# Performance work log

Measured on AMD Instinct MI355X. Metric: run time of the kernel, lower is better.

## Reference

```python
import jax, jax.numpy as jnp
import numpy as np

N_ATOMS = 400000   # total atoms in batch
N_MODELS = 4       # number of elements / sub-models
N_POINTS = 512     # inducing points per GPR
N_DESC = 32        # descriptor length


def setup_inputs() -> dict:
    key = jax.random.key(0)
    k1, k2, k3, k4 = jax.random.split(key, 4)
    element = jax.random.randint(k1, (N_ATOMS,), 0, N_MODELS, dtype=jnp.int32)
    x = jax.random.normal(k2, (N_ATOMS, N_DESC), dtype=jnp.float32)
    inducing_x = jax.random.normal(k3, (N_MODELS, N_POINTS, N_DESC), dtype=jnp.float32)
    alpha = jax.random.normal(k4, (N_MODELS, N_POINTS), dtype=jnp.float32)
    # torch code initializes lengthscales to -1 (log-space) with ARD (one per descriptor)
    log_ls = -jnp.ones((N_MODELS, N_DESC), dtype=jnp.float32)
    return {"element": element, "x": x, "inducing_x": inducing_x,
            "alpha": alpha, "log_ls": log_ls}


def _gpr_energies(x, Zm, am, log_lsm):
    """InducedKernelGPR.forward for one sub-model over ALL atoms.

    dist[p, n] = sum_d (x[n,d] - Z[p,d])^2 / exp(log_ls[d])
    out[n]     = sum_p alpha[p] * exp(-dist[p, n])

    Uses ||a-b||^2 = ||a||^2 + ||b||^2 - 2 a.b on 1/sqrt(ls)-scaled features
    to avoid materializing the [P, N, D] difference tensor.
    """
    inv_sqrt_ls = jnp.exp(-0.5 * log_lsm)          # [D]
    xs = x * inv_sqrt_ls                            # [N, D]
    zs = Zm * inv_sqrt_ls                           # [P, D]
    x2 = jnp.sum(xs * xs, axis=-1)                  # [N]
    z2 = jnp.sum(zs * zs, axis=-1)                  # [P]
    cross = jnp.einsum('pd,nd->pn', zs, xs)         # [P, N]
    dist = z2[:, None] + x2[None, :] - 2.0 * cross  # [P, N]
    return am @ jnp.exp(-dist)                      # [N]


def reference(element, x, inducing_x, alpha, log_ls):
    # Hard routing: each atom gets the prediction of the model matching its element.
    # Loop over the small fixed set of sub-models (structurally distinct params);
    # combine with a mask instead of dynamic-shape gather/scatter (jit-friendly).
    out = jnp.zeros(x.shape[0], dtype=x.dtype)
    for m in range(inducing_x.shape[0]):
        e_m = _gpr_energies(x, inducing_x[m], alpha[m], log_ls[m])  # [N]
        out = jnp.where(element == m, e_m, out)
    return out
```

## Files before the change

### kernel.cpp

```cpp
#include <hip/hip_runtime.h>
#include <math.h>

#define NA 400000
#define NM 4
#define NP 512
#define ND 32
#define SQF 1.6986437f
#define NBH 391
#define GTPB 512
#define NBLK 1024
#define WPM ((NBLK / NM) * 8)
#define ACUT 60.0f

typedef __attribute__((ext_vector_type(8))) _Float16 f16x8;
typedef __attribute__((ext_vector_type(4))) float f32x4;

#define WS_ZH   0
#define WS_AZY  131072
#define WS_BET  139264
#define WS_ISL  147456
#define WS_PART 147968
#define WS_CNT  154224
#define WS_BKT  154240

__global__ void prep_hist_kernel(const float* __restrict__ Z,
                                 const float* __restrict__ alpha,
                                 const float* __restrict__ lls,
                                 const int* __restrict__ el,
                                 unsigned short* __restrict__ zh_w,
                                 float* __restrict__ azy,
                                 float* __restrict__ bet,
                                 float* __restrict__ isl,
                                 int* __restrict__ part)
{
    __shared__ float isl_s[ND];
    __shared__ int h[16][NM];
    int tid = threadIdx.x;
    if (blockIdx.x < NM) {
        int m = blockIdx.x;
        if (tid < ND) {
            float v = expf(-0.5f * lls[m * ND + tid]) * SQF;
            isl_s[tid] = v;
            isl[m * ND + tid] = v;
        }
        __syncthreads();
        for (int p = tid; p < NP; p += blockDim.x) {
            const float* zp = Z + (size_t)(m * NP + p) * ND;
            int t = p >> 4, pl = p & 15;
            size_t fb = (size_t)(m * 32 + t) * 512;
            float z2 = 0.f;
#pragma unroll
            for (int d = 0; d < ND; ++d) {
                float zs = zp[d] * isl_s[d];
                _Float16 zh = (_Float16)zs;
                float zr = (float)zh;
                z2 = fmaf(zr, zr, z2);
                int lane = pl + 16 * (d >> 3), j = d & 7;
                zh_w[fb + lane * 8 + j] = __builtin_bit_cast(unsigned short, zh);
            }
            azy[m * NP + p] = -0.5f * z2;
            bet[m * NP + p] = alpha[m * NP + p] * 8.673617379884035e-19f;
        }
    } else {
        int wnd = blockIdx.x - NM;
        int wv = tid >> 6, lane = tid & 63;
        int i = wnd * 1024 + tid;
        int e = (i < NA) ? el[i] : -1;
#pragma unroll
        for (int mm = 0; mm < NM; ++mm) {
            unsigned long long b = __ballot(e == mm);
            if (lane == 0) h[wv][mm] = __popcll(b);
        }
        __syncthreads();
        if (tid < NM) {
            int s = 0;
#pragma unroll
            for (int k = 0; k < 16; ++k) s += h[k][tid];
            part[wnd * 4 + tid] = s;
        }
    }
}

__global__ void scatter_kernel(const int* __restrict__ el,
                               const int* __restrict__ part,
                               int* __restrict__ cnt,
                               int* __restrict__ bucket)
{
    __shared__ int wcnt_s[16][NM];
    __shared__ int wvoff_s[16][NM];
    __shared__ int gbase_s[NM];
    __shared__ int tot_s[NM];
    __shared__ int bw_s[NM];
    int b = blockIdx.x, tid = threadIdx.x;
    int wv = tid >> 6, lane = tid & 63;
    int i = b * 1024 + tid;
    int e = (i < NA) ? el[i] : -1;
    unsigned long long lt = (1ULL << lane) - 1ULL;
    int myrank = 0;
#pragma unroll
    for (int mm = 0; mm < NM; ++mm) {
        unsigned long long bl = __ballot(e == mm);
        if (e == mm) myrank = __popcll(bl & lt);
        if (lane == 0) wcnt_s[wv][mm] = __popcll(bl);
    }
    if (wv == 0) {
        int t0 = 0, t1 = 0, t2 = 0, t3 = 0, b0 = 0, b1 = 0, b2 = 0, b3 = 0;
        for (int w2 = lane; w2 < NBH; w2 += 64) {
            int4 pv = ((const int4*)part)[w2];
            t0 += pv.x; t1 += pv.y; t2 += pv.z; t3 += pv.w;
            if (w2 < b) { b0 += pv.x; b1 += pv.y; b2 += pv.z; b3 += pv.w; }
        }
#pragma unroll
        for (int s = 1; s < 64; s <<= 1) {
            t0 += __shfl_xor(t0, s); t1 += __shfl_xor(t1, s);
            t2 += __shfl_xor(t2, s); t3 += __shfl_xor(t3, s);
            b0 += __shfl_xor(b0, s); b1 += __shfl_xor(b1, s);
            b2 += __shfl_xor(b2, s); b3 += __shfl_xor(b3, s);
        }
        if (lane == 0) {
            tot_s[0] = t0; tot_s[1] = t1; tot_s[2] = t2; tot_s[3] = t3;
            bw_s[0] = b0; bw_s[1] = b1; bw_s[2] = b2; bw_s[3] = b3;
        }
    }
    __syncthreads();
    if (tid < NM) {
        int g = bw_s[tid];
        for (int mm = 0; mm < NM; ++mm) if (mm < tid) g += tot_s[mm];
        gbase_s[tid] = g;
        int run = 0;
#pragma unroll
        for (int k = 0; k < 16; ++k) { wvoff_s[k][tid] = run; run += wcnt_s[k][tid]; }
        if (b == 0) cnt[tid] = tot_s[tid];
    }
    __syncthreads();
    if (e >= 0) bucket[gbase_s[e] + wvoff_s[wv][e] + myrank] = i;
}

static __device__ __forceinline__ void build_frags(
    const float* __restrict__ x, const int* __restrict__ bucket,
    int base, int c, int wbase, int ll, int k0, float4 w0, float4 w1,
    f16x8* Bh, float* x2lc)
{
#pragma unroll
    for (int nt = 0; nt < 4; ++nt) {
        int j = wbase + nt * 16 + ll;
        int n = bucket[base + ((j < c) ? j : (c - 1))];
        const float4* xp = (const float4*)(x + (size_t)n * ND + k0);
        float4 a = xp[0], b = xp[1];
        float xs[8] = {a.x * w0.x, a.y * w0.y, a.z * w0.z, a.w * w0.w,
                       b.x * w1.x, b.y * w1.y, b.z * w1.z, b.w * w1.w};
        float s2 = 0.f;
#pragma unroll
        for (int i = 0; i < 8; ++i) {
            _Float16 xh = (_Float16)xs[i];
            Bh[nt][i] = xh;
            float xr = (float)xh;
            s2 = fmaf(xr, xr, s2);
        }
        s2 += __shfl_xor(s2, 16);
        s2 += __shfl_xor(s2, 32);
        x2lc[nt] = 0.5f * s2 - ACUT;
    }
}

__global__ __launch_bounds__(GTPB, 4)
void gpr_kernel(const float* __restrict__ x,
                const int* __restrict__ bucket,
                const unsigned short* __restrict__ zh_w,
                const float* __restrict__ azy_w,
                const float* __restrict__ bet_w,
                const float* __restrict__ isl_w,
                const int* __restrict__ cnt_w,
                float* __restrict__ out)
{
    __shared__ __align__(16) unsigned short zf[32][512];
    __shared__ __align__(16) float azy_s[NP];
    __shared__ __align__(16) float bet_s[NP];

    int m = blockIdx.x & 3;
    int tid = threadIdx.x;
    int c0 = cnt_w[0], c1 = cnt_w[1], c2 = cnt_w[2], c3 = cnt_w[3];
    int c    = (m == 0) ? c0 : (m == 1) ? c1 : (m == 2) ? c2 : c3;
    int base = (m == 0) ? 0 : (m == 1) ? c0 : (m == 2) ? c0 + c1 : c0 + c1 + c2;

    int wv = tid >> 6, lane = tid & 63;
    int lg = lane >> 4, ll = lane & 15;
    int k0 = lg * 8;
    int wm = (blockIdx.x >> 2) * 8 + wv;

    const float4* wp = (const float4*)(isl_w + m * ND + k0);
    float4 w0 = wp[0], w1 = wp[1];

    {
        const int4* zg = (const int4*)(zh_w + (size_t)m * 16384);
        int4* zs = (int4*)&zf[0][0];
#pragma unroll
        for (int i = 0; i < 4; ++i) zs[tid + i * GTPB] = zg[tid + i * GTPB];
        if (tid < 128)
            ((float4*)azy_s)[tid] = ((const float4*)(azy_w + m * NP))[tid];
        else if (tid < 256)
            ((float4*)bet_s)[tid - 128] = ((const float4*)(bet_w + m * NP))[tid - 128];
    }

    f16x8 Bh[4];
    float x2lc[4];
    bool active = (wm * 64 < c);
    if (active)
        build_frags(x, bucket, base, c, wm * 64, ll, k0, w0, w1, Bh, x2lc);

    __syncthreads();

    for (int s = wm; s * 64 < c; s += WPM) {
        int wbase = s * 64;
        if (s != wm)
            build_frags(x, bucket, base, c, wbase, ll, k0, w0, w1, Bh, x2lc);

        float acc[4] = {0.f, 0.f, 0.f, 0.f};

        f16x8 Ah = *(const f16x8*)&zf[0][lane * 8];
        float4 di = *(const float4*)&azy_s[4 * lg];
        float4 bi = *(const float4*)&bet_s[4 * lg];

#pragma unroll 2
        for (int t = 0; t < 32; ++t) {
            f16x8 AhC = Ah;
            f32x4 dinit = __builtin_bit_cast(f32x4, di);
            float4 be4 = bi;
            int tn = (t + 1) & 31;
            Ah = *(const f16x8*)&zf[tn][lane * 8];
            di = *(const float4*)&azy_s[tn * 16 + 4 * lg];
            bi = *(const float4*)&bet_s[tn * 16 + 4 * lg];

            f32x4 dd[4];
            __builtin_amdgcn_s_setprio(1);
#pragma unroll
            for (int nt = 0; nt < 4; ++nt)
                dd[nt] = __builtin_amdgcn_mfma_f32_16x16x32_f16(AhC, Bh[nt], dinit, 0, 0, 0);
            __builtin_amdgcn_s_setprio(0);

#pragma unroll
            for (int nt = 0; nt < 4; ++nt) {
                f32x4 d = dd[nt];
                float mx = fmaxf(fmaxf(d[0], d[1]), fmaxf(d[2], d[3]));
                if (__any(mx >= x2lc[nt])) {
                    float xl = x2lc[nt];
                    acc[nt] = fmaf(be4.x, __builtin_amdgcn_exp2f(d[0] - xl), acc[nt]);
                    acc[nt] = fmaf(be4.y, __builtin_amdgcn_exp2f(d[1] - xl), acc[nt]);
                    acc[nt] = fmaf(be4.z, __builtin_amdgcn_exp2f(d[2] - xl), acc[nt]);
                    acc[nt] = fmaf(be4.w, __builtin_amdgcn_exp2f(d[3] - xl), acc[nt]);
                }
            }
        }

#pragma unroll
        for (int nt = 0; nt < 4; ++nt) {
            float v = acc[nt];
            v += __shfl_xor(v, 16);
            v += __shfl_xor(v, 32);
            if (lane < 16) {
                int j = wbase + nt * 16 + lane;
                if (j < c) out[bucket[base + j]] = v;
            }
        }
    }
}

extern "C" void kernel_launch(void* const* d_in, const int* in_sizes, int n_in,
                              void* d_out, int out_size, void* d_ws, size_t ws_size,
                              hipStream_t stream)
{
    const int*   element    = (const int*)d_in[0];
    const float* x          = (const float*)d_in[1];
    const float* inducing_x = (const float*)d_in[2];
    const float* alpha      = (const float*)d_in[3];
    const float* log_ls     = (const float*)d_in[4];
    float* out = (float*)d_out;

    char* ws = (char*)d_ws;
    unsigned short* zh = (unsigned short*)(ws + WS_ZH);
    float* azy  = (float*)(ws + WS_AZY);
    float* bet  = (float*)(ws + WS_BET);
    float* isl  = (float*)(ws + WS_ISL);
    int*   part = (int*)(ws + WS_PART);
    int*   cnt  = (int*)(ws + WS_CNT);
    int*   bkt  = (int*)(ws + WS_BKT);

    (void)in_sizes; (void)n_in; (void)out_size; (void)ws_size;

    prep_hist_kernel<<<NM + NBH, 1024, 0, stream>>>(inducing_x, alpha, log_ls, element,
                                                    zh, azy, bet, isl, part);
    scatter_kernel<<<NBH, 1024, 0, stream>>>(element, part, cnt, bkt);
    gpr_kernel<<<NBLK, GTPB, 0, stream>>>(x, bkt, zh, azy, bet, isl, cnt, out);
}
```

Measured before the change: 44.01 us.

## Process 16-atom subtiles sequentially with software-prefetched x loads

Restructures the per-wave work so that, instead of holding four 16-atom B fragments and issuing four MFMAs per inducing-point step, each wave handles one 16-atom subtile at a time. The x row for the next subtile is prefetched into registers while the current one runs its 32-step MFMA/exp loop. This cuts register pressure and hides gather latency. In exchange each MFMA now has to wait on its own dependent exp chain, and the LDS reads of Z, azy and beta are repeated four times per 64-atom tile.

```diff
diff --git a/kernel.cpp b/kernel.cpp
--- a/kernel.cpp
+++ b/kernel.cpp
@@ -136,33 +136,6 @@
     if (e >= 0) bucket[gbase_s[e] + wvoff_s[wv][e] + myrank] = i;
 }
 
-static __device__ __forceinline__ void build_frags(
-    const float* __restrict__ x, const int* __restrict__ bucket,
-    int base, int c, int wbase, int ll, int k0, float4 w0, float4 w1,
-    f16x8* Bh, float* x2lc)
-{
-#pragma unroll
-    for (int nt = 0; nt < 4; ++nt) {
-        int j = wbase + nt * 16 + ll;
-        int n = bucket[base + ((j < c) ? j : (c - 1))];
-        const float4* xp = (const float4*)(x + (size_t)n * ND + k0);
-        float4 a = xp[0], b = xp[1];
-        float xs[8] = {a.x * w0.x, a.y * w0.y, a.z * w0.z, a.w * w0.w,
-                       b.x * w1.x, b.y * w1.y, b.z * w1.z, b.w * w1.w};
-        float s2 = 0.f;
-#pragma unroll
-        for (int i = 0; i < 8; ++i) {
-            _Float16 xh = (_Float16)xs[i];
-            Bh[nt][i] = xh;
-            float xr = (float)xh;
-            s2 = fmaf(xr, xr, s2);
-        }
-        s2 += __shfl_xor(s2, 16);
-        s2 += __shfl_xor(s2, 32);
-        x2lc[nt] = 0.5f * s2 - ACUT;
-    }
-}
-
 __global__ __launch_bounds__(GTPB, 4)
 void gpr_kernel(const float* __restrict__ x,
                 const int* __restrict__ bucket,
@@ -202,59 +175,75 @@
             ((float4*)bet_s)[tid - 128] = ((const float4*)(bet_w + m * NP))[tid - 128];
     }
 
-    f16x8 Bh[4];
-    float x2lc[4];
+    float4 ra, rb;
     bool active = (wm * 64 < c);
-    if (active)
-        build_frags(x, bucket, base, c, wm * 64, ll, k0, w0, w1, Bh, x2lc);
+    if (active) {
+        int j = wm * 64 + ll;
+        int n = bucket[base + ((j < c) ? j : (c - 1))];
+        const float4* xp = (const float4*)(x + (size_t)n * ND + k0);
+        ra = xp[0]; rb = xp[1];
+    }
 
     __syncthreads();
 
     for (int s = wm; s * 64 < c; s += WPM) {
         int wbase = s * 64;
-        if (s != wm)
-            build_frags(x, bucket, base, c, wbase, ll, k0, w0, w1, Bh, x2lc);
-
-        float acc[4] = {0.f, 0.f, 0.f, 0.f};
-
-        f16x8 Ah = *(const f16x8*)&zf[0][lane * 8];
-        float4 di = *(const float4*)&azy_s[4 * lg];
-        float4 bi = *(const float4*)&bet_s[4 * lg];
+        if (s != wm) {
+            int j = wbase + ll;
+            int n = bucket[base + ((j < c) ? j : (c - 1))];
+            const float4* xp = (const float4*)(x + (size_t)n * ND + k0);
+            ra = xp[0]; rb = xp[1];
+        }
+
+        for (int nt = 0; nt < 4; ++nt) {
+            float xs[8] = {ra.x * w0.x, ra.y * w0.y, ra.z * w0.z, ra.w * w0.w,
+                           rb.x * w1.x, rb.y * w1.y, rb.z * w1.z, rb.w * w1.w};
+            f16x8 B;
+            float s2 = 0.f;
+#pragma unroll
+            for (int i = 0; i < 8; ++i) {
+                _Float16 xh = (_Float16)xs[i];
+                B[i] = xh;
+                float xr = (float)xh;
+                s2 = fmaf(xr, xr, s2);
+            }
+            s2 += __shfl_xor(s2, 16);
+            s2 += __shfl_xor(s2, 32);
+            float x2lc = 0.5f * s2 - ACUT;
+
+            if (nt < 3) {
+                int j = wbase + (nt + 1) * 16 + ll;
+                int n = bucket[base + ((j < c) ? j : (c - 1))];
+                const float4* xp = (const float4*)(x + (size_t)n * ND + k0);
+                ra = xp[0]; rb = xp[1];
+            }
+
+            float acc = 0.f;
+            f16x8 Ah = *(const f16x8*)&zf[0][lane * 8];
+            float4 di = *(const float4*)&azy_s[4 * lg];
+            float4 bi = *(const float4*)&bet_s[4 * lg];
 
 #pragma unroll 2
-        for (int t = 0; t < 32; ++t) {
-            f16x8 AhC = Ah;
-            f32x4 dinit = __builtin_bit_cast(f32x4, di);
-            float4 be4 = bi;
-            int tn = (t + 1) & 31;
-            Ah = *(const f16x8*)&zf[tn][lane * 8];
-            di = *(const float4*)&azy_s[tn * 16 + 4 * lg];
-            bi = *(const float4*)&bet_s[tn * 16 + 4 * lg];
-
-            f32x4 dd[4];
-            __builtin_amdgcn_s_setprio(1);
-#pragma unroll
-            for (int nt = 0; nt < 4; ++nt)
-                dd[nt] = __builtin_amdgcn_mfma_f32_16x16x32_f16(AhC, Bh[nt], dinit, 0, 0, 0);
-            __builtin_amdgcn_s_setprio(0);
-
-#pragma unroll
-            for (int nt = 0; nt < 4; ++nt) {
-                f32x4 d = dd[nt];
+            for (int t = 0; t < 32; ++t) {
+                f16x8 AhC = Ah;
+                f32x4 dinit = __builtin_bit_cast(f32x4, di);
+                float4 be4 = bi;
+                int tn = (t + 1) & 31;
+                Ah = *(const f16x8*)&zf[tn][lane * 8];
+                di = *(const float4*)&azy_s[tn * 16 + 4 * lg];
+                bi = *(const float4*)&bet_s[tn * 16 + 4 * lg];
+
+                f32x4 d = __builtin_amdgcn_mfma_f32_16x16x32_f16(AhC, B, dinit, 0, 0, 0);
                 float mx = fmaxf(fmaxf(d[0], d[1]), fmaxf(d[2], d[3]));
-                if (__any(mx >= x2lc[nt])) {
-                    float xl = x2lc[nt];
-                    acc[nt] = fmaf(be4.x, __builtin_amdgcn_exp2f(d[0] - xl), acc[nt]);
-                    acc[nt] = fmaf(be4.y, __builtin_amdgcn_exp2f(d[1] - xl), acc[nt]);
-                    acc[nt] = fmaf(be4.z, __builtin_amdgcn_exp2f(d[2] - xl), acc[nt]);
-                    acc[nt] = fmaf(be4.w, __builtin_amdgcn_exp2f(d[3] - xl), acc[nt]);
+                if (__any(mx >= x2lc)) {
+                    acc = fmaf(be4.x, __builtin_amdgcn_exp2f(d[0] - x2lc), acc);
+                    acc = fmaf(be4.y, __builtin_amdgcn_exp2f(d[1] - x2lc), acc);
+                    acc = fmaf(be4.z, __builtin_amdgcn_exp2f(d[2] - x2lc), acc);
+                    acc = fmaf(be4.w, __builtin_amdgcn_exp2f(d[3] - x2lc), acc);
                 }
             }
-        }
-
-#pragma unroll
-        for (int nt = 0; nt < 4; ++nt) {
-            float v = acc[nt];
+
+            float v = acc;
             v += __shfl_xor(v, 16);
             v += __shfl_xor(v, 32);
             if (lane < 16) {
```

New measurement: 47.96 us. 1.09x slower.
